# Kernel tuning notes

Hardware: AMD Instinct MI355X
Metric: run time of the kernel (lower is better)

Reference implementation:

```python
import jax, jax.numpy as jnp
import numpy as np

B, NB, BS, K = 16, 512, 128, 32
N = NB * BS
GRAPH_WEIGHT = 0.3


def setup_inputs() -> dict:
    key = jax.random.key(0)
    k1, k2, k3, k4, k5 = jax.random.split(key, 5)
    logits = jax.random.normal(k1, (B, N, 1), dtype=jnp.float32)
    targets = jax.random.bernoulli(k2, 0.5, (B, N)).astype(jnp.float32)[..., None]
    r = jax.random.uniform(k3, (B, N))
    sup_mask = r < 0.10
    ignore_mask = (r >= 0.10) & (r < 0.20)
    kv_indices = jax.random.randint(k4, (B, NB, K), 0, NB).astype(jnp.int32)
    kv_num_blocks = jax.random.randint(k5, (B, NB), 0, K + 1).astype(jnp.int32)
    return {
        "logits": logits,
        "targets": targets,
        "sup_mask": sup_mask,
        "ignore_mask": ignore_mask,
        "kv_indices": kv_indices,
        "kv_num_blocks": kv_num_blocks,
        "block_size": BS,
    }


def _bce_masked_mean(x, t, m):
    # numerically stable BCE-with-logits, mean over masked entries
    per = jnp.maximum(x, 0.0) - x * t + jnp.log1p(jnp.exp(-jnp.abs(x)))
    mf = m.astype(x.dtype)
    cnt = mf.sum()
    return (per * mf).sum() / jnp.maximum(cnt, 1.0)


def _graph_smoothness(logits, sup_mask, ignore_mask, kv_indices, kv_num_blocks, block_size):
    b, n = sup_mask.shape
    nb = n // block_size
    probs = jax.nn.sigmoid(logits[..., 0])                 # [B, N]
    pb = probs.reshape(b, nb, block_size)                  # [B, NB, BS]
    unc = (~ignore_mask & ~sup_mask).reshape(b, nb, block_size)  # uncertain q nodes
    vld = (~ignore_mask).reshape(b, nb, block_size)        # valid neighbor nodes

    bidx = jnp.arange(b)[:, None, None]
    neigh_p = pb[bidx, kv_indices]                         # [B, NB, K, BS]
    neigh_v = vld[bidx, kv_indices]                        # [B, NB, K, BS]
    k = kv_indices.shape[-1]
    slot_ok = jnp.arange(k)[None, None, :] < kv_num_blocks[:, :, None]  # [B, NB, K]
    nmask = (neigh_v & slot_ok[..., None]).astype(probs.dtype)          # [B, NB, K, BS]

    cnt = nmask.sum(axis=(-1, -2))                         # [B, NB] neighbor counts
    nmean = (neigh_p * nmask).sum(axis=(-1, -2)) / jnp.maximum(cnt, 1.0)

    q_unc_cnt = unc.sum(axis=-1)                           # [B, NB]
    block_ok = (q_unc_cnt > 0) & (kv_num_blocks > 0) & (cnt > 0)
    sq = (((pb - nmean[..., None]) ** 2) * unc.astype(probs.dtype)).sum(-1)  # [B, NB]
    loss_b = jnp.where(block_ok, sq, 0.0).sum(-1)          # [B]
    n_unc_b = jnp.where(block_ok, q_unc_cnt, 0).sum(-1).astype(probs.dtype)  # [B]
    batch_ok = n_unc_b > 0
    per_batch = jnp.where(batch_ok, loss_b / jnp.maximum(n_unc_b, 1.0), 0.0)
    n_valid = batch_ok.sum().astype(probs.dtype)
    return per_batch.sum() / jnp.maximum(n_valid, 1.0)


def reference(logits, targets, sup_mask, ignore_mask, kv_indices, kv_num_blocks, block_size):
    loss_sup = _bce_masked_mean(logits[..., 0], targets[..., 0], sup_mask)
    loss_graph = _graph_smoothness(logits, sup_mask, ignore_mask,
                                   kv_indices, kv_num_blocks, block_size)
    return loss_sup + GRAPH_WEIGHT * loss_graph
```

## Files before the change

### kernel.cpp

```cpp
#include <hip/hip_runtime.h>
#include <math.h>

#define BB 16
#define NBB 512
#define BSS 128
#define KK 32
#define NBLK (BB*NBB)
#define STATS_GRID 1024


#define VC_OFF 0
#define SU_OFF 16384
#define BC_OFF 49152
#define P_OFF  65536
#define TICKET_OFF 65570

__global__ __launch_bounds__(256) void stats_kernel(
    const float* __restrict__ logits, const float* __restrict__ targets,
    const unsigned char* __restrict__ sup_b, const unsigned char* __restrict__ ign_b,
    float* __restrict__ W)
{
    const int t = threadIdx.x;
    __shared__ int s_mode;
    if (t == 0) s_mode = 0;
    __syncthreads();
    int local = 0;
    #pragma unroll
    for (int r = 0; r < 4; ++r) {
        if (sup_b[4 * (t + 256 * r) + 1] != 0) local = 1;
    }
    if (local) atomicOr(&s_mode, 1);
    __syncthreads();
    const bool byteMode = (s_mode != 0);

    const int gid = blockIdx.x * 256 + t;
    const float4 x4 = ((const float4*)logits)[gid];
    const float4 t4 = ((const float4*)targets)[gid];
    bool s[4], g[4];
    if (byteMode) {
        const unsigned int sm = ((const unsigned int*)sup_b)[gid];
        const unsigned int gm = ((const unsigned int*)ign_b)[gid];
        #pragma unroll
        for (int j = 0; j < 4; ++j) {
            s[j] = ((sm >> (8 * j)) & 0xffu) != 0;
            g[j] = ((gm >> (8 * j)) & 0xffu) != 0;
        }
    } else {
        const int4 sm = ((const int4*)sup_b)[gid];
        const int4 gm = ((const int4*)ign_b)[gid];
        s[0] = sm.x != 0; s[1] = sm.y != 0; s[2] = sm.z != 0; s[3] = sm.w != 0;
        g[0] = gm.x != 0; g[1] = gm.y != 0; g[2] = gm.z != 0; g[3] = gm.w != 0;
    }
    const float xs[4] = {x4.x, x4.y, x4.z, x4.w};
    const float ts[4] = {t4.x, t4.y, t4.z, t4.w};

    float svp = 0.f, cv = 0.f, su = 0.f, su2 = 0.f, cu = 0.f, bs = 0.f, bc = 0.f;
    #pragma unroll
    for (int j = 0; j < 4; ++j) {
        const float x = xs[j];
        const float p = 1.0f / (1.0f + expf(-x));
        if (s[j]) {
            bs += fmaxf(x, 0.0f) - x * ts[j] + log1pf(expf(-fabsf(x)));
            bc += 1.0f;
        }
        if (!g[j]) {
            svp += p; cv += 1.0f;
            if (!s[j]) { su += p; su2 += p * p; cu += 1.0f; }
        }
    }
    #pragma unroll
    for (int off = 16; off > 0; off >>= 1) {
        svp += __shfl_down(svp, off, 32);
        cv  += __shfl_down(cv,  off, 32);
        su  += __shfl_down(su,  off, 32);
        su2 += __shfl_down(su2, off, 32);
        cu  += __shfl_down(cu,  off, 32);
        bs  += __shfl_down(bs,  off, 32);
        bc  += __shfl_down(bc,  off, 32);
    }
    if ((t & 31) == 0) {
        const int qb = blockIdx.x * 8 + (t >> 5);
        ((float2*)(W + VC_OFF))[qb] = make_float2(svp, cv);
        ((float4*)(W + SU_OFF))[qb] = make_float4(su, su2, cu, 0.0f);
        ((float2*)(W + BC_OFF))[qb] = make_float2(bs, bc);
    }
    if (blockIdx.x == 0 && t == 0) {
        #pragma unroll
        for (int i = 0; i < 34; ++i) W[P_OFF + i] = 0.0f;
        *((int*)(W + TICKET_OFF)) = 0;
    }
}

__global__ __launch_bounds__(256) void graph_kernel(
    const int* __restrict__ kv_idx, const int* __restrict__ kv_nb,
    float* __restrict__ W, float* __restrict__ out)
{
    const int t    = threadIdx.x;
    const int grp  = t >> 5;
    const int slot = t & 31;
    const int b    = blockIdx.x >> 4;

    const float2* __restrict__ VC  = (const float2*)(W + VC_OFF);
    const float4* __restrict__ SU  = (const float4*)(W + SU_OFF);
    const float2* __restrict__ BCp = (const float2*)(W + BC_OFF);
    float* P    = W + P_OFF;
    int* ticket = (int*)(W + TICKET_OFF);
    const float2* __restrict__ VCb = VC + (b << 9);

    float loss_a = 0.f, nunc_a = 0.f, bs_a = 0.f, bc_a = 0.f;
    #pragma unroll
    for (int qq = 0; qq < 4; ++qq) {
        const int gb  = blockIdx.x * 32 + grp * 4 + qq;
        const int knb = kv_nb[gb];
        float psum = 0.f, cnt = 0.f;
        if (slot < knb) {
            const int j = kv_idx[(size_t)gb * KK + slot];
            const float2 vc = VCb[j];
            psum = vc.x; cnt = vc.y;
        }
        #pragma unroll
        for (int m = 16; m > 0; m >>= 1) {
            psum += __shfl_xor(psum, m, 32);
            cnt  += __shfl_xor(cnt,  m, 32);
        }
        if (slot == 0) {
            const float4 su  = SU[gb];
            const float2 bcv = BCp[gb];
            bs_a += bcv.x; bc_a += bcv.y;
            if (su.z > 0.0f && knb > 0 && cnt > 0.0f) {
                const float mm = psum / fmaxf(cnt, 1.0f);
                loss_a += su.y - 2.0f * mm * su.x + mm * mm * su.z;
                nunc_a += su.z;
            }
        }
    }

    __shared__ float s[8][4];
    if (slot == 0) {
        s[grp][0] = loss_a; s[grp][1] = nunc_a;
        s[grp][2] = bs_a;   s[grp][3] = bc_a;
    }
    __syncthreads();
    if (t == 0) {
        float l = 0.f, n = 0.f, bs = 0.f, bc = 0.f;
        #pragma unroll
        for (int g = 0; g < 8; ++g) {
            l += s[g][0]; n += s[g][1]; bs += s[g][2]; bc += s[g][3];
        }
        atomicAdd(&P[b * 2 + 0], l);
        atomicAdd(&P[b * 2 + 1], n);
        atomicAdd(&P[32], bs);
        atomicAdd(&P[33], bc);
        __threadfence();
        const int rank = atomicAdd(ticket, 1);
        if (rank == 255) {
            __threadfence();
            float gsum = 0.f, nval = 0.f;
            for (int b2 = 0; b2 < BB; ++b2) {
                const float lv = atomicAdd(&P[b2 * 2 + 0], 0.0f);
                const float nv = atomicAdd(&P[b2 * 2 + 1], 0.0f);
                if (nv > 0.0f) { gsum += lv / fmaxf(nv, 1.0f); nval += 1.0f; }
            }
            const float tbs = atomicAdd(&P[32], 0.0f);
            const float tbc = atomicAdd(&P[33], 0.0f);
            out[0] = tbs / fmaxf(tbc, 1.0f) + 0.3f * (gsum / fmaxf(nval, 1.0f));
        }
    }
}

extern "C" void kernel_launch(void* const* d_in, const int* in_sizes, int n_in,
                              void* d_out, int out_size, void* d_ws, size_t ws_size,
                              hipStream_t stream) {
    (void)in_sizes; (void)n_in; (void)out_size; (void)ws_size;
    const float* logits  = (const float*)d_in[0];
    const float* targets = (const float*)d_in[1];
    const unsigned char* supm = (const unsigned char*)d_in[2];
    const unsigned char* ignm = (const unsigned char*)d_in[3];
    const int* kv_idx = (const int*)d_in[4];
    const int* kv_nb  = (const int*)d_in[5];
    float* W   = (float*)d_ws;
    float* out = (float*)d_out;

    hipLaunchKernelGGL(stats_kernel, dim3(STATS_GRID), dim3(256), 0, stream,
                       logits, targets, supm, ignm, W);
    hipLaunchKernelGGL(graph_kernel, dim3(256), dim3(256), 0, stream,
                       kv_idx, kv_nb, W, out);
}
```

Measured before the change: 106.9 us.

## Spread graph reduction over more blocks with per-batch atomic tickets

The graph kernel now launches 1024 blocks, and each warp handles one query block instead of four, which is meant to expose more parallelism for the latency-bound gather. The global single-counter atomics are replaced by per-batch partial sums and tickets, followed by a second-level ticket over the 16 batches. This spreads atomic contention across addresses, at the cost of more launched blocks and a two-level finalization.

Result: slower. 140.4 us (+31.3%).

```diff
diff --git a/kernel.cpp b/kernel.cpp
--- a/kernel.cpp
+++ b/kernel.cpp
@@ -13,7 +13,7 @@
 #define SU_OFF 16384
 #define BC_OFF 49152
 #define P_OFF  65536
-#define TICKET_OFF 65570
+#define TICKET_OFF 65600
 
 __global__ __launch_bounds__(256) void stats_kernel(
     const float* __restrict__ logits, const float* __restrict__ targets,
@@ -84,11 +84,8 @@
         ((float4*)(W + SU_OFF))[qb] = make_float4(su, su2, cu, 0.0f);
         ((float2*)(W + BC_OFF))[qb] = make_float2(bs, bc);
     }
-    if (blockIdx.x == 0 && t == 0) {
-        #pragma unroll
-        for (int i = 0; i < 34; ++i) W[P_OFF + i] = 0.0f;
-        *((int*)(W + TICKET_OFF)) = 0;
-    }
+    if (blockIdx.x == 0 && t < 64) W[P_OFF + t] = 0.0f;
+    if (blockIdx.x == 0 && t < 17) ((int*)(W + TICKET_OFF))[t] = 0;
 }
 
 __global__ __launch_bounds__(256) void graph_kernel(
@@ -98,72 +95,73 @@
     const int t    = threadIdx.x;
     const int grp  = t >> 5;
     const int slot = t & 31;
-    const int b    = blockIdx.x >> 4;
+    const int gb   = blockIdx.x * 8 + grp;
+    const int b    = blockIdx.x >> 6;
 
     const float2* __restrict__ VC  = (const float2*)(W + VC_OFF);
     const float4* __restrict__ SU  = (const float4*)(W + SU_OFF);
     const float2* __restrict__ BCp = (const float2*)(W + BC_OFF);
-    float* P    = W + P_OFF;
-    int* ticket = (int*)(W + TICKET_OFF);
-    const float2* __restrict__ VCb = VC + (b << 9);
+    float* P      = W + P_OFF;
+    int* btick    = (int*)(W + TICKET_OFF);
+    int* gtick    = btick + 16;
 
-    float loss_a = 0.f, nunc_a = 0.f, bs_a = 0.f, bc_a = 0.f;
+    const int knb = kv_nb[gb];
+    float psum = 0.f, cnt = 0.f;
+    if (slot < knb) {
+        const int j = kv_idx[(size_t)gb * KK + slot];
+        const float2 vc = VC[(b << 9) + j];
+        psum = vc.x; cnt = vc.y;
+    }
     #pragma unroll
-    for (int qq = 0; qq < 4; ++qq) {
-        const int gb  = blockIdx.x * 32 + grp * 4 + qq;
-        const int knb = kv_nb[gb];
-        float psum = 0.f, cnt = 0.f;
-        if (slot < knb) {
-            const int j = kv_idx[(size_t)gb * KK + slot];
-            const float2 vc = VCb[j];
-            psum = vc.x; cnt = vc.y;
-        }
-        #pragma unroll
-        for (int m = 16; m > 0; m >>= 1) {
-            psum += __shfl_xor(psum, m, 32);
-            cnt  += __shfl_xor(cnt,  m, 32);
-        }
-        if (slot == 0) {
-            const float4 su  = SU[gb];
-            const float2 bcv = BCp[gb];
-            bs_a += bcv.x; bc_a += bcv.y;
-            if (su.z > 0.0f && knb > 0 && cnt > 0.0f) {
-                const float mm = psum / fmaxf(cnt, 1.0f);
-                loss_a += su.y - 2.0f * mm * su.x + mm * mm * su.z;
-                nunc_a += su.z;
-            }
+    for (int m = 16; m > 0; m >>= 1) {
+        psum += __shfl_xor(psum, m, 32);
+        cnt  += __shfl_xor(cnt,  m, 32);
+    }
+
+    float loss = 0.f, nunc = 0.f, bs = 0.f, bc = 0.f;
+    if (slot == 0) {
+        const float4 su  = SU[gb];
+        const float2 bcv = BCp[gb];
+        bs = bcv.x; bc = bcv.y;
+        if (su.z > 0.0f && knb > 0 && cnt > 0.0f) {
+            const float mm = psum / fmaxf(cnt, 1.0f);
+            loss = su.y - 2.0f * mm * su.x + mm * mm * su.z;
+            nunc = su.z;
         }
     }
 
     __shared__ float s[8][4];
     if (slot == 0) {
-        s[grp][0] = loss_a; s[grp][1] = nunc_a;
-        s[grp][2] = bs_a;   s[grp][3] = bc_a;
+        s[grp][0] = loss; s[grp][1] = nunc; s[grp][2] = bs; s[grp][3] = bc;
     }
     __syncthreads();
     if (t == 0) {
-        float l = 0.f, n = 0.f, bs = 0.f, bc = 0.f;
+        float l = 0.f, n = 0.f, b2s = 0.f, b2c = 0.f;
         #pragma unroll
         for (int g = 0; g < 8; ++g) {
-            l += s[g][0]; n += s[g][1]; bs += s[g][2]; bc += s[g][3];
+            l += s[g][0]; n += s[g][1]; b2s += s[g][2]; b2c += s[g][3];
         }
-        atomicAdd(&P[b * 2 + 0], l);
-        atomicAdd(&P[b * 2 + 1], n);
-        atomicAdd(&P[32], bs);
-        atomicAdd(&P[33], bc);
+        atomicAdd(&P[b * 4 + 0], l);
+        atomicAdd(&P[b * 4 + 1], n);
+        atomicAdd(&P[b * 4 + 2], b2s);
+        atomicAdd(&P[b * 4 + 3], b2c);
         __threadfence();
-        const int rank = atomicAdd(ticket, 1);
-        if (rank == 255) {
+        const int brank = atomicAdd(&btick[b], 1);
+        if (brank == 63) {
             __threadfence();
-            float gsum = 0.f, nval = 0.f;
-            for (int b2 = 0; b2 < BB; ++b2) {
-                const float lv = atomicAdd(&P[b2 * 2 + 0], 0.0f);
-                const float nv = atomicAdd(&P[b2 * 2 + 1], 0.0f);
-                if (nv > 0.0f) { gsum += lv / fmaxf(nv, 1.0f); nval += 1.0f; }
+            const int grank = atomicAdd(gtick, 1);
+            if (grank == 15) {
+                __threadfence();
+                float gsum = 0.f, nval = 0.f, tbs = 0.f, tbc = 0.f;
+                for (int b2 = 0; b2 < BB; ++b2) {
+                    const float lv = atomicAdd(&P[b2 * 4 + 0], 0.0f);
+                    const float nv = atomicAdd(&P[b2 * 4 + 1], 0.0f);
+                    tbs += atomicAdd(&P[b2 * 4 + 2], 0.0f);
+                    tbc += atomicAdd(&P[b2 * 4 + 3], 0.0f);
+                    if (nv > 0.0f) { gsum += lv / fmaxf(nv, 1.0f); nval += 1.0f; }
+                }
+                out[0] = tbs / fmaxf(tbc, 1.0f) + 0.3f * (gsum / fmaxf(nval, 1.0f));
             }
-            const float tbs = atomicAdd(&P[32], 0.0f);
-            const float tbc = atomicAdd(&P[33], 0.0f);
-            out[0] = tbs / fmaxf(tbc, 1.0f) + 0.3f * (gsum / fmaxf(nval, 1.0f));
         }
     }
 }
@@ -183,6 +181,6 @@
 
     hipLaunchKernelGGL(stats_kernel, dim3(STATS_GRID), dim3(256), 0, stream,
                        logits, targets, supm, ignm, W);
-    hipLaunchKernelGGL(graph_kernel, dim3(256), dim3(256), 0, stream,
+    hipLaunchKernelGGL(graph_kernel, dim3(1024), dim3(256), 0, stream,
                        kv_idx, kv_nb, W, out);
 }
```
